# Optimization experiments

Measured on AMD Instinct MI355X. Metric: run time of the kernel, lower is better.

## Reference

```python
import jax, jax.numpy as jnp
import numpy as np

HEAD_SIZE = 128
BLOCK_SIZE = 2048


def setup_inputs() -> dict:
    key = jax.random.key(0)
    kx, kk, kq, kv = jax.random.split(key, 4)
    B, T, C = 8, 2048, HEAD_SIZE
    s = 1.0 / np.sqrt(C)
    x = jax.random.normal(kx, (B, T, C), dtype=jnp.float32)
    Wk = jax.random.normal(kk, (C, C), dtype=jnp.float32) * s
    Wq = jax.random.normal(kq, (C, C), dtype=jnp.float32) * s
    Wv = jax.random.normal(kv, (C, C), dtype=jnp.float32) * s
    return {"x": x, "Wk": Wk, "Wq": Wq, "Wv": Wv}


def reference(x, Wk, Wq, Wv):
    B, T, C = x.shape
    # nn.Linear(C, C, bias=False): y = x @ W.T
    k = jnp.einsum('btc,dc->btd', x, Wk)
    q = jnp.einsum('btc,dc->btd', x, Wq)
    v = jnp.einsum('btc,dc->btd', x, Wv)
    scores = jnp.einsum('btd,bsd->bts', q, k) * (C ** -0.5)  # [B,T,T]
    causal = jnp.tril(jnp.ones((T, T), dtype=bool))
    scores = jnp.where(causal, scores, -jnp.inf)
    weights = jax.nn.softmax(scores, axis=-1)
    return jnp.einsum('bts,bsd->btd', weights, v)
```

## Files before the change

### kernel.cpp

```cpp
#include <hip/hip_runtime.h>

#define T_SEQ 2048
#define C_DIM 128
#define S_QK 0.08838834764831845f

typedef __attribute__((ext_vector_type(8))) short bf16x8;
typedef __attribute__((ext_vector_type(4))) short bf16x4;
typedef __attribute__((ext_vector_type(4))) float f32x4;
typedef __attribute__((ext_vector_type(2))) unsigned int u32x2;

#define OPART_OFF 12582912UL
#define ML_OFF    43778048UL

#define GLOAD_LDS16(gp, lp)                                          \
    __builtin_amdgcn_global_load_lds(                                \
        (const __attribute__((address_space(1))) void*)(gp),         \
        (__attribute__((address_space(3))) void*)(lp), 16, 0, 0)

__device__ __forceinline__ unsigned short f2bf(float f) {
    union { float f; unsigned int u; } v; v.f = f;
    unsigned int r = v.u + 0x7FFFu + ((v.u >> 16) & 1u);
    return (unsigned short)(r >> 16);
}

__device__ __forceinline__ f32x4 mfma16(bf16x4 a, bf16x4 b, f32x4 c) {
    f32x4 d = c;
    asm("v_mfma_f32_16x16x16_bf16 %0, %1, %2, %0" : "+v"(d) : "v"(a), "v"(b));
    return d;
}

__device__ __forceinline__ int base5(int qt) {
    int g = qt / 5 + 1;
    return 5 * g * (g - 1) / 2 + (qt - 5 * (g - 1)) * g;
}

__global__ __launch_bounds__(256) void proj_kernel(
    const float* __restrict__ x,
    const float* __restrict__ Wk, const float* __restrict__ Wq,
    const float* __restrict__ Wv,
    unsigned short* __restrict__ qo, unsigned short* __restrict__ ko,
    unsigned short* __restrict__ vto)
{
    const int rt = blockIdx.x;
    const int z  = blockIdx.y;
    const int tid  = threadIdx.x;
    const int lane = tid & 63;
    const int w    = tid >> 6;
    const int n16  = lane & 15;
    const int quad = lane >> 4;

    __shared__ __align__(16) unsigned short Wl[128 * 136];
    __shared__ __align__(16) unsigned short Xl[9216];

    const float* Wsrc = (z == 0 ? Wq : z == 1 ? Wk : Wv);
    const float wscale = (z == 0) ? S_QK : 1.0f;
    #pragma unroll
    for (int i = 0; i < 16; ++i) {
        int e = (tid + i * 256) * 4;
        int r = e >> 7, c = e & 127;
        float4 v = *reinterpret_cast<const float4*>(Wsrc + e);
        float ax = v.x * wscale, ay = v.y * wscale;
        float az = v.z * wscale, aw = v.w * wscale;
        unsigned lo, hi;
        asm("v_cvt_pk_bf16_f32 %0, %1, %2" : "=v"(lo) : "v"(ax), "v"(ay));
        asm("v_cvt_pk_bf16_f32 %0, %1, %2" : "=v"(hi) : "v"(az), "v"(aw));
        uint2 o2; o2.x = lo; o2.y = hi;
        *reinterpret_cast<uint2*>(&Wl[r * 136 + c]) = o2;
    }
    const float* xrow = x + (size_t)rt * 64 * C_DIM;
    #pragma unroll
    for (int i = 0; i < 8; ++i) {
        int e = (tid + i * 256) * 4;
        int r = e >> 7, c = e & 127;
        float4 v = *reinterpret_cast<const float4*>(xrow + e);
        unsigned lo, hi;
        asm("v_cvt_pk_bf16_f32 %0, %1, %2" : "=v"(lo) : "v"(v.x), "v"(v.y));
        asm("v_cvt_pk_bf16_f32 %0, %1, %2" : "=v"(hi) : "v"(v.z), "v"(v.w));
        uint2 o2; o2.x = lo; o2.y = hi;
        *reinterpret_cast<uint2*>(&Xl[r * 136 + c]) = o2;
    }
    __syncthreads();

    const int arow = w * 16 + n16;
    bf16x8 afr[4];
    #pragma unroll
    for (int kk = 0; kk < 4; ++kk)
        afr[kk] = *reinterpret_cast<const bf16x8*>(&Xl[arow * 136 + kk * 32 + quad * 8]);

    f32x4 acc[8];
    #pragma unroll
    for (int nt = 0; nt < 8; ++nt) acc[nt] = (f32x4){0.f, 0.f, 0.f, 0.f};
    #pragma unroll
    for (int kk = 0; kk < 4; ++kk)
        #pragma unroll
        for (int nt = 0; nt < 8; ++nt) {
            bf16x8 bfr = *reinterpret_cast<const bf16x8*>(
                &Wl[(nt * 16 + n16) * 136 + kk * 32 + quad * 8]);
            acc[nt] = __builtin_amdgcn_mfma_f32_16x16x32_bf16(afr[kk], bfr, acc[nt], 0, 0, 0);
        }

    const int trow_base = w * 16 + quad * 4;
    __syncthreads();
    if (z < 2) {
        #pragma unroll
        for (int nt = 0; nt < 8; ++nt)
            #pragma unroll
            for (int r = 0; r < 4; ++r)
                Xl[(trow_base + r) * 136 + nt * 16 + n16] = f2bf(acc[nt][r]);
        __syncthreads();
        unsigned short* dst = (z == 0 ? qo : ko) + (size_t)rt * 64 * C_DIM;
        #pragma unroll
        for (int i = 0; i < 4; ++i) {
            int e = (tid + i * 256) * 8;
            int r = e >> 7, c = e & 127;
            *reinterpret_cast<uint4*>(dst + e) =
                *reinterpret_cast<const uint4*>(&Xl[r * 136 + c]);
        }
    } else {
        const int b  = rt >> 5;
        const int qt = rt & 31;
        #pragma unroll
        for (int nt = 0; nt < 8; ++nt)
            #pragma unroll
            for (int r = 0; r < 4; ++r)
                Xl[(nt * 16 + n16) * 72 + trow_base + r] = f2bf(acc[nt][r]);
        __syncthreads();
        unsigned short* dst = vto + (size_t)b * C_DIM * T_SEQ + (size_t)qt * 64;
        #pragma unroll
        for (int i = 0; i < 4; ++i) {
            int e = tid + i * 256;
            int d = e >> 3, cv = (e & 7) * 8;
            *reinterpret_cast<uint4*>(dst + (size_t)d * T_SEQ + cv) =
                *reinterpret_cast<const uint4*>(&Xl[d * 72 + cv]);
        }
    }
}

__device__ __forceinline__ void stage_tile32(
    const char* ksb, const char* vsb,
    unsigned short* klbuf, unsigned short* vlbuf, int tid, int w)
{
    #pragma unroll
    for (int it = 0; it < 2; ++it) {
        const int L = it * 256 + tid;
        const int r = L >> 4, c = L & 15;
        GLOAD_LDS16(ksb + r * 256 + ((c ^ (r & 7)) << 4),
                    klbuf + (size_t)(it * 256 + w * 64) * 8);
    }
    #pragma unroll
    for (int it = 0; it < 2; ++it) {
        const int L = it * 256 + tid;
        const int r = L >> 2, c = L & 3;
        GLOAD_LDS16(vsb + (size_t)r * (T_SEQ * 2) +
                        ((c ^ (r & 3) ^ ((r >> 2) & 3)) << 4),
                    vlbuf + (size_t)(it * 256 + w * 64) * 8);
    }
}

__global__ __launch_bounds__(256, 3) void attn_kernel(
    const unsigned short* __restrict__ qb,
    const unsigned short* __restrict__ kb,
    const unsigned short* __restrict__ vtb,
    float* __restrict__ opart, float2* __restrict__ mlbuf,
    float* __restrict__ out)
{
    const int lin = blockIdx.x;
    const int b   = lin & 7;
    const int s   = lin >> 3;
    int g = 1, gbase = 0;
    while (s - gbase >= 5 * g) { gbase += 5 * g; ++g; }
    const int qt    = 5 * (g - 1) + (s - gbase) / g;
    const int chunk = (s - gbase) % g;
    const int nch   = g;

    const int tid  = threadIdx.x;
    const int lane = tid & 63;
    const int w    = tid >> 6;
    const int n16  = lane & 15;
    const int quad = lane >> 4;

    __shared__ __align__(16) unsigned short Kl[2][32 * 128];
    __shared__ __align__(16) unsigned short Vl[2][128 * 32];

    const size_t bT = (size_t)b * T_SEQ;
    const int qbase = qt * 64 + w * 16;
    const int ulim  = 4 * qt + w;

    const int st0 = chunk * 10;
    const int st1 = min(st0 + 10, 2 * qt + 2);

    const char* kbase = (const char*)(kb + bT * C_DIM);
    const char* vbase = (const char*)(vtb + (size_t)b * C_DIM * T_SEQ);

    stage_tile32(kbase + (size_t)st0 * 8192, vbase + (size_t)st0 * 64,
                 Kl[0], Vl[0], tid, w);

    const unsigned short* qp = qb + (bT + qbase + n16) * C_DIM + quad * 8;
    bf16x8 qfr0 = *reinterpret_cast<const bf16x8*>(qp);
    bf16x8 qfr1 = *reinterpret_cast<const bf16x8*>(qp + 32);
    bf16x8 qfr2 = *reinterpret_cast<const bf16x8*>(qp + 64);
    bf16x8 qfr3 = *reinterpret_cast<const bf16x8*>(qp + 96);

    f32x4 o0 = (f32x4){0.f,0.f,0.f,0.f}, o1 = (f32x4){0.f,0.f,0.f,0.f};
    f32x4 o2 = (f32x4){0.f,0.f,0.f,0.f}, o3 = (f32x4){0.f,0.f,0.f,0.f};
    f32x4 o4 = (f32x4){0.f,0.f,0.f,0.f}, o5 = (f32x4){0.f,0.f,0.f,0.f};
    f32x4 o6 = (f32x4){0.f,0.f,0.f,0.f}, o7 = (f32x4){0.f,0.f,0.f,0.f};
    float l_ = 0.f;

    const int kx  = n16 & 7;
    const int sig = (n16 & 3) ^ ((n16 >> 2) & 3);
    const int vof0 = n16 * 32 + (((quad >> 1) ^ sig) << 3) + (quad & 1) * 4;
    const int vof1 = n16 * 32 + ((((quad >> 1) + 2) ^ sig) << 3) + (quad & 1) * 4;

    int cur = 0;
    for (int st = st0; st < st1; ++st, cur ^= 1) {
        if (st + 1 < st1) {
            stage_tile32(kbase + (size_t)(st + 1) * 8192,
                         vbase + (size_t)(st + 1) * 64,
                         Kl[cur ^ 1], Vl[cur ^ 1], tid, w);
            asm volatile("s_waitcnt vmcnt(4)" ::: "memory");
        } else {
            asm volatile("s_waitcnt vmcnt(0)" ::: "memory");
        }
        __builtin_amdgcn_s_barrier();

        const unsigned short* klc = Kl[cur];
        const unsigned short* vlc = Vl[cur];

        #pragma unroll
        for (int sub = 0; sub < 2; ++sub) {
            const int u = st * 2 + sub;
            if (u <= ulim) {
                const unsigned short* krow = klc + (sub * 16 + n16) * 128;
                bf16x8 kf0 = *reinterpret_cast<const bf16x8*>(krow + (((0 + quad) ^ kx) << 3));
                bf16x8 kf1 = *reinterpret_cast<const bf16x8*>(krow + (((4 + quad) ^ kx) << 3));
                bf16x8 kf2 = *reinterpret_cast<const bf16x8*>(krow + (((8 + quad) ^ kx) << 3));
                bf16x8 kf3 = *reinterpret_cast<const bf16x8*>(krow + (((12 + quad) ^ kx) << 3));
                f32x4 s4 = (f32x4){0.f, 0.f, 0.f, 0.f};
                s4 = __builtin_amdgcn_mfma_f32_16x16x32_bf16(kf0, qfr0, s4, 0, 0, 0);
                s4 = __builtin_amdgcn_mfma_f32_16x16x32_bf16(kf1, qfr1, s4, 0, 0, 0);
                s4 = __builtin_amdgcn_mfma_f32_16x16x32_bf16(kf2, qfr2, s4, 0, 0, 0);
                s4 = __builtin_amdgcn_mfma_f32_16x16x32_bf16(kf3, qfr3, s4, 0, 0, 0);

                if (u == ulim) {
                    #pragma unroll
                    for (int r = 0; r < 4; ++r) {
                        int sabs = u * 16 + quad * 4 + r;
                        if (sabs > qbase + n16) s4[r] = -1e30f;
                    }
                }

                float p0 = __expf(s4[0]), p1 = __expf(s4[1]);
                float p2 = __expf(s4[2]), p3 = __expf(s4[3]);
                l_ += (p0 + p1) + (p2 + p3);

                unsigned plo, phi;
                asm("v_cvt_pk_bf16_f32 %0, %1, %2" : "=v"(plo) : "v"(p0), "v"(p1));
                asm("v_cvt_pk_bf16_f32 %0, %1, %2" : "=v"(phi) : "v"(p2), "v"(p3));
                u32x2 pp; pp.x = plo; pp.y = phi;
                bf16x4 pv = __builtin_bit_cast(bf16x4, pp);

                const int vof = sub ? vof1 : vof0;
                o0 = mfma16(*reinterpret_cast<const bf16x4*>(vlc + 0 * 512 + vof), pv, o0);
                o1 = mfma16(*reinterpret_cast<const bf16x4*>(vlc + 1 * 512 + vof), pv, o1);
                o2 = mfma16(*reinterpret_cast<const bf16x4*>(vlc + 2 * 512 + vof), pv, o2);
                o3 = mfma16(*reinterpret_cast<const bf16x4*>(vlc + 3 * 512 + vof), pv, o3);
                o4 = mfma16(*reinterpret_cast<const bf16x4*>(vlc + 4 * 512 + vof), pv, o4);
                o5 = mfma16(*reinterpret_cast<const bf16x4*>(vlc + 5 * 512 + vof), pv, o5);
                o6 = mfma16(*reinterpret_cast<const bf16x4*>(vlc + 6 * 512 + vof), pv, o6);
                o7 = mfma16(*reinterpret_cast<const bf16x4*>(vlc + 7 * 512 + vof), pv, o7);
            }
        }

        asm volatile("s_waitcnt lgkmcnt(0)" ::: "memory");
        __builtin_amdgcn_s_barrier();
    }

    l_ += __shfl_xor(l_, 16);
    l_ += __shfl_xor(l_, 32);

#define STORE4(dst, o, sc)                                            \
    { float4 r4;                                                      \
      r4.x = (o)[0] * (sc); r4.y = (o)[1] * (sc);                     \
      r4.z = (o)[2] * (sc); r4.w = (o)[3] * (sc);                     \
      *reinterpret_cast<float4*>(dst) = r4; }

    if (nch == 1) {
        float* outp = out + (bT + qbase + n16) * C_DIM + quad * 4;
        const float inv = 1.0f / l_;
        STORE4(outp +   0, o0, inv); STORE4(outp +  16, o1, inv);
        STORE4(outp +  32, o2, inv); STORE4(outp +  48, o3, inv);
        STORE4(outp +  64, o4, inv); STORE4(outp +  80, o5, inv);
        STORE4(outp +  96, o6, inv); STORE4(outp + 112, o7, inv);
        return;
    }

    const int slot = b * 119 + s;
    float* op = opart + (size_t)slot * 8192 + (size_t)(w * 16 + n16) * 128 + quad * 4;
    STORE4(op +   0, o0, 1.0f); STORE4(op +  16, o1, 1.0f);
    STORE4(op +  32, o2, 1.0f); STORE4(op +  48, o3, 1.0f);
    STORE4(op +  64, o4, 1.0f); STORE4(op +  80, o5, 1.0f);
    STORE4(op +  96, o6, 1.0f); STORE4(op + 112, o7, 1.0f);
    if (quad == 0)
        mlbuf[(size_t)slot * 64 + w * 16 + n16] = make_float2(0.f, l_);
#undef STORE4
}

__global__ __launch_bounds__(256) void merge_kernel(
    const float* __restrict__ opart, const float2* __restrict__ mlbuf,
    float* __restrict__ out)
{
    const int qt = 5 + blockIdx.x;
    const int b  = blockIdx.y;
    const int nch  = qt / 5 + 1;
    const int base = b * 119 + base5(qt);
    const int row = threadIdx.x >> 2;
    const int c0  = (threadIdx.x & 3) * 32;

    float L = 0.f;
    #pragma unroll
    for (int i = 0; i < 7; ++i)
        if (i < nch) L += mlbuf[(size_t)(base + i) * 64 + row].y;
    const float inv = 1.0f / L;

    float* orow = out + ((size_t)(b * T_SEQ + qt * 64 + row)) * C_DIM;
    #pragma unroll
    for (int j = 0; j < 8; ++j) {
        int col = c0 + j * 4;
        float ax = 0.f, ay = 0.f, az = 0.f, aw = 0.f;
        #pragma unroll
        for (int i = 0; i < 7; ++i) {
            if (i < nch) {
                float4 p = *reinterpret_cast<const float4*>(
                    opart + (size_t)(base + i) * 8192 + row * 128 + col);
                ax += p.x; ay += p.y; az += p.z; aw += p.w;
            }
        }
        float4 r4; r4.x = ax * inv; r4.y = ay * inv; r4.z = az * inv; r4.w = aw * inv;
        *reinterpret_cast<float4*>(orow + col) = r4;
    }
}

extern "C" void kernel_launch(void* const* d_in, const int* in_sizes, int n_in,
                              void* d_out, int out_size, void* d_ws, size_t ws_size,
                              hipStream_t stream) {
    const float* x  = (const float*)d_in[0];
    const float* Wk = (const float*)d_in[1];
    const float* Wq = (const float*)d_in[2];
    const float* Wv = (const float*)d_in[3];

    unsigned short* qw  = (unsigned short*)d_ws;
    unsigned short* kw  = qw + 2097152;
    unsigned short* vw  = kw + 2097152;
    float*          opart = (float*)((char*)d_ws + OPART_OFF);
    float2*         mlb   = (float2*)((char*)d_ws + ML_OFF);

    proj_kernel<<<dim3(256, 3), 256, 0, stream>>>(x, Wk, Wq, Wv, qw, kw, vw);
    attn_kernel<<<dim3(952), 256, 0, stream>>>(qw, kw, vw, opart, mlb, (float*)d_out);
    merge_kernel<<<dim3(27, 8), 256, 0, stream>>>(opart, mlb, (float*)d_out);
}
```

Measured before the change: 116.5 us.

## Double query rows per wave to reuse each staged K/V tile twice

Each wave now handles two 16-row query groups, so a block covers 128 query rows instead of 64. Every K/V tile staged in shared memory and read into registers then feeds twice the MFMA work, halving K/V traffic per query. The split-KV chunking, partial-output slots and merge kernel are recomputed for the new tiling, which also cuts the grid to 488 blocks. In exchange, register pressure roughly doubles (16 accumulators plus 8 Q fragments), which can hurt the 3-blocks-per-SIMD occupancy target, and the causal work is balanced less finely.

New measurement: 126.5 us. 8.6% more time.

```diff
diff --git a/kernel.cpp b/kernel.cpp
--- a/kernel.cpp
+++ b/kernel.cpp
@@ -10,7 +10,7 @@
 typedef __attribute__((ext_vector_type(2))) unsigned int u32x2;
 
 #define OPART_OFF 12582912UL
-#define ML_OFF    43778048UL
+#define ML_OFF    44564480UL
 
 #define GLOAD_LDS16(gp, lp)                                          \
     __builtin_amdgcn_global_load_lds(                                \
@@ -27,11 +27,6 @@
     f32x4 d = c;
     asm("v_mfma_f32_16x16x16_bf16 %0, %1, %2, %0" : "+v"(d) : "v"(a), "v"(b));
     return d;
-}
-
-__device__ __forceinline__ int base5(int qt) {
-    int g = qt / 5 + 1;
-    return 5 * g * (g - 1) / 2 + (qt - 5 * (g - 1)) * g;
 }
 
 __global__ __launch_bounds__(256) void proj_kernel(
@@ -167,11 +162,13 @@
     const int lin = blockIdx.x;
     const int b   = lin & 7;
     const int s   = lin >> 3;
-    int g = 1, gbase = 0;
-    while (s - gbase >= 5 * g) { gbase += 5 * g; ++g; }
-    const int qt    = 5 * (g - 1) + (s - gbase) / g;
-    const int chunk = (s - gbase) % g;
-    const int nch   = g;
+    int qt2 = 0, acc = 0, nch = 1;
+    for (;;) {
+        nch = (4 * qt2 + 13) / 10;
+        if (s < acc + nch) break;
+        acc += nch; ++qt2;
+    }
+    const int chunk = s - acc;
 
     const int tid  = threadIdx.x;
     const int lane = tid & 63;
@@ -183,11 +180,14 @@
     __shared__ __align__(16) unsigned short Vl[2][128 * 32];
 
     const size_t bT = (size_t)b * T_SEQ;
-    const int qbase = qt * 64 + w * 16;
-    const int ulim  = 4 * qt + w;
+    const int qbase = qt2 * 128 + w * 32;
+    const int qrA = qbase + n16;
+    const int qrB = qrA + 16;
+    const int uA = 8 * qt2 + 2 * w;
+    const int uB = uA + 1;
 
     const int st0 = chunk * 10;
-    const int st1 = min(st0 + 10, 2 * qt + 2);
+    const int st1 = min(st0 + 10, 4 * qt2 + 4);
 
     const char* kbase = (const char*)(kb + bT * C_DIM);
     const char* vbase = (const char*)(vtb + (size_t)b * C_DIM * T_SEQ);
@@ -195,17 +195,25 @@
     stage_tile32(kbase + (size_t)st0 * 8192, vbase + (size_t)st0 * 64,
                  Kl[0], Vl[0], tid, w);
 
-    const unsigned short* qp = qb + (bT + qbase + n16) * C_DIM + quad * 8;
-    bf16x8 qfr0 = *reinterpret_cast<const bf16x8*>(qp);
-    bf16x8 qfr1 = *reinterpret_cast<const bf16x8*>(qp + 32);
-    bf16x8 qfr2 = *reinterpret_cast<const bf16x8*>(qp + 64);
-    bf16x8 qfr3 = *reinterpret_cast<const bf16x8*>(qp + 96);
-
-    f32x4 o0 = (f32x4){0.f,0.f,0.f,0.f}, o1 = (f32x4){0.f,0.f,0.f,0.f};
-    f32x4 o2 = (f32x4){0.f,0.f,0.f,0.f}, o3 = (f32x4){0.f,0.f,0.f,0.f};
-    f32x4 o4 = (f32x4){0.f,0.f,0.f,0.f}, o5 = (f32x4){0.f,0.f,0.f,0.f};
-    f32x4 o6 = (f32x4){0.f,0.f,0.f,0.f}, o7 = (f32x4){0.f,0.f,0.f,0.f};
-    float l_ = 0.f;
+    const unsigned short* qp = qb + (bT + qrA) * C_DIM + quad * 8;
+    bf16x8 qfrA0 = *reinterpret_cast<const bf16x8*>(qp);
+    bf16x8 qfrA1 = *reinterpret_cast<const bf16x8*>(qp + 32);
+    bf16x8 qfrA2 = *reinterpret_cast<const bf16x8*>(qp + 64);
+    bf16x8 qfrA3 = *reinterpret_cast<const bf16x8*>(qp + 96);
+    bf16x8 qfrB0 = *reinterpret_cast<const bf16x8*>(qp + 16 * C_DIM);
+    bf16x8 qfrB1 = *reinterpret_cast<const bf16x8*>(qp + 16 * C_DIM + 32);
+    bf16x8 qfrB2 = *reinterpret_cast<const bf16x8*>(qp + 16 * C_DIM + 64);
+    bf16x8 qfrB3 = *reinterpret_cast<const bf16x8*>(qp + 16 * C_DIM + 96);
+
+    f32x4 oA0 = (f32x4){0.f,0.f,0.f,0.f}, oA1 = (f32x4){0.f,0.f,0.f,0.f};
+    f32x4 oA2 = (f32x4){0.f,0.f,0.f,0.f}, oA3 = (f32x4){0.f,0.f,0.f,0.f};
+    f32x4 oA4 = (f32x4){0.f,0.f,0.f,0.f}, oA5 = (f32x4){0.f,0.f,0.f,0.f};
+    f32x4 oA6 = (f32x4){0.f,0.f,0.f,0.f}, oA7 = (f32x4){0.f,0.f,0.f,0.f};
+    f32x4 oB0 = (f32x4){0.f,0.f,0.f,0.f}, oB1 = (f32x4){0.f,0.f,0.f,0.f};
+    f32x4 oB2 = (f32x4){0.f,0.f,0.f,0.f}, oB3 = (f32x4){0.f,0.f,0.f,0.f};
+    f32x4 oB4 = (f32x4){0.f,0.f,0.f,0.f}, oB5 = (f32x4){0.f,0.f,0.f,0.f};
+    f32x4 oB6 = (f32x4){0.f,0.f,0.f,0.f}, oB7 = (f32x4){0.f,0.f,0.f,0.f};
+    float lA = 0.f, lB = 0.f;
 
     const int kx  = n16 & 7;
     const int sig = (n16 & 3) ^ ((n16 >> 2) & 3);
@@ -230,45 +238,68 @@
         #pragma unroll
         for (int sub = 0; sub < 2; ++sub) {
             const int u = st * 2 + sub;
-            if (u <= ulim) {
+            if (u <= uB) {
                 const unsigned short* krow = klc + (sub * 16 + n16) * 128;
                 bf16x8 kf0 = *reinterpret_cast<const bf16x8*>(krow + (((0 + quad) ^ kx) << 3));
                 bf16x8 kf1 = *reinterpret_cast<const bf16x8*>(krow + (((4 + quad) ^ kx) << 3));
                 bf16x8 kf2 = *reinterpret_cast<const bf16x8*>(krow + (((8 + quad) ^ kx) << 3));
                 bf16x8 kf3 = *reinterpret_cast<const bf16x8*>(krow + (((12 + quad) ^ kx) << 3));
-                f32x4 s4 = (f32x4){0.f, 0.f, 0.f, 0.f};
-                s4 = __builtin_amdgcn_mfma_f32_16x16x32_bf16(kf0, qfr0, s4, 0, 0, 0);
-                s4 = __builtin_amdgcn_mfma_f32_16x16x32_bf16(kf1, qfr1, s4, 0, 0, 0);
-                s4 = __builtin_amdgcn_mfma_f32_16x16x32_bf16(kf2, qfr2, s4, 0, 0, 0);
-                s4 = __builtin_amdgcn_mfma_f32_16x16x32_bf16(kf3, qfr3, s4, 0, 0, 0);
-
-                if (u == ulim) {
+                const int vof = sub ? vof1 : vof0;
+                const int sb0 = u * 16 + quad * 4;
+
+                if (u <= uA) {
+                    f32x4 s4 = (f32x4){0.f, 0.f, 0.f, 0.f};
+                    s4 = __builtin_amdgcn_mfma_f32_16x16x32_bf16(kf0, qfrA0, s4, 0, 0, 0);
+                    s4 = __builtin_amdgcn_mfma_f32_16x16x32_bf16(kf1, qfrA1, s4, 0, 0, 0);
+                    s4 = __builtin_amdgcn_mfma_f32_16x16x32_bf16(kf2, qfrA2, s4, 0, 0, 0);
+                    s4 = __builtin_amdgcn_mfma_f32_16x16x32_bf16(kf3, qfrA3, s4, 0, 0, 0);
                     #pragma unroll
-                    for (int r = 0; r < 4; ++r) {
-                        int sabs = u * 16 + quad * 4 + r;
-                        if (sabs > qbase + n16) s4[r] = -1e30f;
-                    }
+                    for (int r = 0; r < 4; ++r)
+                        if (sb0 + r > qrA) s4[r] = -1e30f;
+                    float p0 = __expf(s4[0]), p1 = __expf(s4[1]);
+                    float p2 = __expf(s4[2]), p3 = __expf(s4[3]);
+                    lA += (p0 + p1) + (p2 + p3);
+                    unsigned plo, phi;
+                    asm("v_cvt_pk_bf16_f32 %0, %1, %2" : "=v"(plo) : "v"(p0), "v"(p1));
+                    asm("v_cvt_pk_bf16_f32 %0, %1, %2" : "=v"(phi) : "v"(p2), "v"(p3));
+                    u32x2 pp; pp.x = plo; pp.y = phi;
+                    bf16x4 pv = __builtin_bit_cast(bf16x4, pp);
+                    oA0 = mfma16(*reinterpret_cast<const bf16x4*>(vlc + 0 * 512 + vof), pv, oA0);
+                    oA1 = mfma16(*reinterpret_cast<const bf16x4*>(vlc + 1 * 512 + vof), pv, oA1);
+                    oA2 = mfma16(*reinterpret_cast<const bf16x4*>(vlc + 2 * 512 + vof), pv, oA2);
+                    oA3 = mfma16(*reinterpret_cast<const bf16x4*>(vlc + 3 * 512 + vof), pv, oA3);
+                    oA4 = mfma16(*reinterpret_cast<const bf16x4*>(vlc + 4 * 512 + vof), pv, oA4);
+                    oA5 = mfma16(*reinterpret_cast<const bf16x4*>(vlc + 5 * 512 + vof), pv, oA5);
+                    oA6 = mfma16(*reinterpret_cast<const bf16x4*>(vlc + 6 * 512 + vof), pv, oA6);
+                    oA7 = mfma16(*reinterpret_cast<const bf16x4*>(vlc + 7 * 512 + vof), pv, oA7);
                 }
 
-                float p0 = __expf(s4[0]), p1 = __expf(s4[1]);
-                float p2 = __expf(s4[2]), p3 = __expf(s4[3]);
-                l_ += (p0 + p1) + (p2 + p3);
-
-                unsigned plo, phi;
-                asm("v_cvt_pk_bf16_f32 %0, %1, %2" : "=v"(plo) : "v"(p0), "v"(p1));
-                asm("v_cvt_pk_bf16_f32 %0, %1, %2" : "=v"(phi) : "v"(p2), "v"(p3));
-                u32x2 pp; pp.x = plo; pp.y = phi;
-                bf16x4 pv = __builtin_bit_cast(bf16x4, pp);
-
-                const int vof = sub ? vof1 : vof0;
-                o0 = mfma16(*reinterpret_cast<const bf16x4*>(vlc + 0 * 512 + vof), pv, o0);
-                o1 = mfma16(*reinterpret_cast<const bf16x4*>(vlc + 1 * 512 + vof), pv, o1);
-                o2 = mfma16(*reinterpret_cast<const bf16x4*>(vlc + 2 * 512 + vof), pv, o2);
-                o3 = mfma16(*reinterpret_cast<const bf16x4*>(vlc + 3 * 512 + vof), pv, o3);
-                o4 = mfma16(*reinterpret_cast<const bf16x4*>(vlc + 4 * 512 + vof), pv, o4);
-                o5 = mfma16(*reinterpret_cast<const bf16x4*>(vlc + 5 * 512 + vof), pv, o5);
-                o6 = mfma16(*reinterpret_cast<const bf16x4*>(vlc + 6 * 512 + vof), pv, o6);
-                o7 = mfma16(*reinterpret_cast<const bf16x4*>(vlc + 7 * 512 + vof), pv, o7);
+                {
+                    f32x4 s4 = (f32x4){0.f, 0.f, 0.f, 0.f};
+                    s4 = __builtin_amdgcn_mfma_f32_16x16x32_bf16(kf0, qfrB0, s4, 0, 0, 0);
+                    s4 = __builtin_amdgcn_mfma_f32_16x16x32_bf16(kf1, qfrB1, s4, 0, 0, 0);
+                    s4 = __builtin_amdgcn_mfma_f32_16x16x32_bf16(kf2, qfrB2, s4, 0, 0, 0);
+                    s4 = __builtin_amdgcn_mfma_f32_16x16x32_bf16(kf3, qfrB3, s4, 0, 0, 0);
+                    #pragma unroll
+                    for (int r = 0; r < 4; ++r)
+                        if (sb0 + r > qrB) s4[r] = -1e30f;
+                    float p0 = __expf(s4[0]), p1 = __expf(s4[1]);
+                    float p2 = __expf(s4[2]), p3 = __expf(s4[3]);
+                    lB += (p0 + p1) + (p2 + p3);
+                    unsigned plo, phi;
+                    asm("v_cvt_pk_bf16_f32 %0, %1, %2" : "=v"(plo) : "v"(p0), "v"(p1));
+                    asm("v_cvt_pk_bf16_f32 %0, %1, %2" : "=v"(phi) : "v"(p2), "v"(p3));
+                    u32x2 pp; pp.x = plo; pp.y = phi;
+                    bf16x4 pv = __builtin_bit_cast(bf16x4, pp);
+                    oB0 = mfma16(*reinterpret_cast<const bf16x4*>(vlc + 0 * 512 + vof), pv, oB0);
+                    oB1 = mfma16(*reinterpret_cast<const bf16x4*>(vlc + 1 * 512 + vof), pv, oB1);
+                    oB2 = mfma16(*reinterpret_cast<const bf16x4*>(vlc + 2 * 512 + vof), pv, oB2);
+                    oB3 = mfma16(*reinterpret_cast<const bf16x4*>(vlc + 3 * 512 + vof), pv, oB3);
+                    oB4 = mfma16(*reinterpret_cast<const bf16x4*>(vlc + 4 * 512 + vof), pv, oB4);
+                    oB5 = mfma16(*reinterpret_cast<const bf16x4*>(vlc + 5 * 512 + vof), pv, oB5);
+                    oB6 = mfma16(*reinterpret_cast<const bf16x4*>(vlc + 6 * 512 + vof), pv, oB6);
+                    oB7 = mfma16(*reinterpret_cast<const bf16x4*>(vlc + 7 * 512 + vof), pv, oB7);
+                }
             }
         }
 
@@ -276,8 +307,8 @@
         __builtin_amdgcn_s_barrier();
     }
 
-    l_ += __shfl_xor(l_, 16);
-    l_ += __shfl_xor(l_, 32);
+    lA += __shfl_xor(lA, 16); lA += __shfl_xor(lA, 32);
+    lB += __shfl_xor(lB, 16); lB += __shfl_xor(lB, 32);
 
 #define STORE4(dst, o, sc)                                            \
     { float4 r4;                                                      \
@@ -286,23 +317,36 @@
       *reinterpret_cast<float4*>(dst) = r4; }
 
     if (nch == 1) {
-        float* outp = out + (bT + qbase + n16) * C_DIM + quad * 4;
-        const float inv = 1.0f / l_;
-        STORE4(outp +   0, o0, inv); STORE4(outp +  16, o1, inv);
-        STORE4(outp +  32, o2, inv); STORE4(outp +  48, o3, inv);
-        STORE4(outp +  64, o4, inv); STORE4(outp +  80, o5, inv);
-        STORE4(outp +  96, o6, inv); STORE4(outp + 112, o7, inv);
+        float* oa = out + (bT + qrA) * C_DIM + quad * 4;
+        float* ob = oa + 16 * C_DIM;
+        const float invA = 1.0f / lA, invB = 1.0f / lB;
+        STORE4(oa +   0, oA0, invA); STORE4(oa +  16, oA1, invA);
+        STORE4(oa +  32, oA2, invA); STORE4(oa +  48, oA3, invA);
+        STORE4(oa +  64, oA4, invA); STORE4(oa +  80, oA5, invA);
+        STORE4(oa +  96, oA6, invA); STORE4(oa + 112, oA7, invA);
+        STORE4(ob +   0, oB0, invB); STORE4(ob +  16, oB1, invB);
+        STORE4(ob +  32, oB2, invB); STORE4(ob +  48, oB3, invB);
+        STORE4(ob +  64, oB4, invB); STORE4(ob +  80, oB5, invB);
+        STORE4(ob +  96, oB6, invB); STORE4(ob + 112, oB7, invB);
         return;
     }
 
-    const int slot = b * 119 + s;
-    float* op = opart + (size_t)slot * 8192 + (size_t)(w * 16 + n16) * 128 + quad * 4;
-    STORE4(op +   0, o0, 1.0f); STORE4(op +  16, o1, 1.0f);
-    STORE4(op +  32, o2, 1.0f); STORE4(op +  48, o3, 1.0f);
-    STORE4(op +  64, o4, 1.0f); STORE4(op +  80, o5, 1.0f);
-    STORE4(op +  96, o6, 1.0f); STORE4(op + 112, o7, 1.0f);
-    if (quad == 0)
-        mlbuf[(size_t)slot * 64 + w * 16 + n16] = make_float2(0.f, l_);
+    const int slot = b * 61 + s;
+    float* opa = opart + (size_t)slot * 16384
+                 + (size_t)(w * 32 + n16) * 128 + quad * 4;
+    float* opb = opa + 16 * 128;
+    STORE4(opa +   0, oA0, 1.0f); STORE4(opa +  16, oA1, 1.0f);
+    STORE4(opa +  32, oA2, 1.0f); STORE4(opa +  48, oA3, 1.0f);
+    STORE4(opa +  64, oA4, 1.0f); STORE4(opa +  80, oA5, 1.0f);
+    STORE4(opa +  96, oA6, 1.0f); STORE4(opa + 112, oA7, 1.0f);
+    STORE4(opb +   0, oB0, 1.0f); STORE4(opb +  16, oB1, 1.0f);
+    STORE4(opb +  32, oB2, 1.0f); STORE4(opb +  48, oB3, 1.0f);
+    STORE4(opb +  64, oB4, 1.0f); STORE4(opb +  80, oB5, 1.0f);
+    STORE4(opb +  96, oB6, 1.0f); STORE4(opb + 112, oB7, 1.0f);
+    if (quad == 0) {
+        mlbuf[(size_t)slot * 128 + w * 32 + n16]      = make_float2(0.f, lA);
+        mlbuf[(size_t)slot * 128 + w * 32 + 16 + n16] = make_float2(0.f, lB);
+    }
 #undef STORE4
 }
 
@@ -310,29 +354,31 @@
     const float* __restrict__ opart, const float2* __restrict__ mlbuf,
     float* __restrict__ out)
 {
-    const int qt = 5 + blockIdx.x;
-    const int b  = blockIdx.y;
-    const int nch  = qt / 5 + 1;
-    const int base = b * 119 + base5(qt);
-    const int row = threadIdx.x >> 2;
-    const int c0  = (threadIdx.x & 3) * 32;
+    const int qt2 = 2 + blockIdx.x;
+    const int b   = blockIdx.y;
+    const int nch = (4 * qt2 + 13) / 10;
+    int sb = 0;
+    for (int j = 0; j < qt2; ++j) sb += (4 * j + 13) / 10;
+    const int base = b * 61 + sb;
+    const int row = threadIdx.x >> 1;
+    const int c0  = (threadIdx.x & 1) * 64;
 
     float L = 0.f;
     #pragma unroll
     for (int i = 0; i < 7; ++i)
-        if (i < nch) L += mlbuf[(size_t)(base + i) * 64 + row].y;
+        if (i < nch) L += mlbuf[(size_t)(base + i) * 128 + row].y;
     const float inv = 1.0f / L;
 
-    float* orow = out + ((size_t)(b * T_SEQ + qt * 64 + row)) * C_DIM;
-    #pragma unroll
-    for (int j = 0; j < 8; ++j) {
+    float* orow = out + ((size_t)(b * T_SEQ + qt2 * 128 + row)) * C_DIM;
+    #pragma unroll
+    for (int j = 0; j < 16; ++j) {
         int col = c0 + j * 4;
         float ax = 0.f, ay = 0.f, az = 0.f, aw = 0.f;
         #pragma unroll
         for (int i = 0; i < 7; ++i) {
             if (i < nch) {
                 float4 p = *reinterpret_cast<const float4*>(
-                    opart + (size_t)(base + i) * 8192 + row * 128 + col);
+                    opart + (size_t)(base + i) * 16384 + row * 128 + col);
                 ax += p.x; ay += p.y; az += p.z; aw += p.w;
             }
         }
@@ -356,6 +402,6 @@
     float2*         mlb   = (float2*)((char*)d_ws + ML_OFF);
 
     proj_kernel<<<dim3(256, 3), 256, 0, stream>>>(x, Wk, Wq, Wv, qw, kw, vw);
-    attn_kernel<<<dim3(952), 256, 0, stream>>>(qw, kw, vw, opart, mlb, (float*)d_out);
-    merge_kernel<<<dim3(27, 8), 256, 0, stream>>>(opart, mlb, (float*)d_out);
-}
+    attn_kernel<<<dim3(488), 256, 0, stream>>>(qw, kw, vw, opart, mlb, (float*)d_out);
+    merge_kernel<<<dim3(14, 8), 256, 0, stream>>>(opart, mlb, (float*)d_out);
+}
```

## Switch attention to single-wave 16-row blocks with 16-tile KV split chunks

Applied to the files above, without the earlier changes.

Attention now runs as 64-thread workgroups, each handling 16 query rows, instead of 256-thread blocks covering 64 rows with four waves. KV is consumed in 16-key tiles double-buffered per wave, and work is split into chunks of up to 16 tiles, giving 4608 blocks. This removes block-wide barriers and the idle waves left by causal imbalance. In exchange, each K/V tile is staged per wave rather than shared across four waves, and there are more partial outputs to merge.

Result: slower. 130.3 us (+11.9%).

```diff
diff --git a/kernel.cpp b/kernel.cpp
--- a/kernel.cpp
+++ b/kernel.cpp
@@ -10,7 +10,7 @@
 typedef __attribute__((ext_vector_type(2))) unsigned int u32x2;
 
 #define OPART_OFF 12582912UL
-#define ML_OFF    43778048UL
+#define ML_OFF    50331648UL
 
 #define GLOAD_LDS16(gp, lp)                                          \
     __builtin_amdgcn_global_load_lds(                                \
@@ -27,11 +27,6 @@
     f32x4 d = c;
     asm("v_mfma_f32_16x16x16_bf16 %0, %1, %2, %0" : "+v"(d) : "v"(a), "v"(b));
     return d;
-}
-
-__device__ __forceinline__ int base5(int qt) {
-    int g = qt / 5 + 1;
-    return 5 * g * (g - 1) / 2 + (qt - 5 * (g - 1)) * g;
 }
 
 __global__ __launch_bounds__(256) void proj_kernel(
@@ -136,28 +131,27 @@
     }
 }
 
-__device__ __forceinline__ void stage_tile32(
+__device__ __forceinline__ void stage16(
     const char* ksb, const char* vsb,
-    unsigned short* klbuf, unsigned short* vlbuf, int tid, int w)
+    unsigned short* kl, unsigned short* vl, int tid)
 {
     #pragma unroll
-    for (int it = 0; it < 2; ++it) {
-        const int L = it * 256 + tid;
+    for (int it = 0; it < 4; ++it) {
+        const int L = it * 64 + tid;
         const int r = L >> 4, c = L & 15;
         GLOAD_LDS16(ksb + r * 256 + ((c ^ (r & 7)) << 4),
-                    klbuf + (size_t)(it * 256 + w * 64) * 8);
-    }
-    #pragma unroll
-    for (int it = 0; it < 2; ++it) {
-        const int L = it * 256 + tid;
-        const int r = L >> 2, c = L & 3;
-        GLOAD_LDS16(vsb + (size_t)r * (T_SEQ * 2) +
-                        ((c ^ (r & 3) ^ ((r >> 2) & 3)) << 4),
-                    vlbuf + (size_t)(it * 256 + w * 64) * 8);
-    }
-}
-
-__global__ __launch_bounds__(256, 3) void attn_kernel(
+                    kl + (size_t)(it * 64) * 8);
+    }
+    #pragma unroll
+    for (int it = 0; it < 4; ++it) {
+        const int L = it * 64 + tid;
+        const int r = L >> 1, c = L & 1;
+        GLOAD_LDS16(vsb + (size_t)r * (T_SEQ * 2) + ((c ^ (r & 1)) << 4),
+                    vl + (size_t)(it * 64) * 8);
+    }
+}
+
+__global__ __launch_bounds__(64, 3) void attn_kernel(
     const unsigned short* __restrict__ qb,
     const unsigned short* __restrict__ kb,
     const unsigned short* __restrict__ vtb,
@@ -167,35 +161,32 @@
     const int lin = blockIdx.x;
     const int b   = lin & 7;
     const int s   = lin >> 3;
-    int g = 1, gbase = 0;
-    while (s - gbase >= 5 * g) { gbase += 5 * g; ++g; }
-    const int qt    = 5 * (g - 1) + (s - gbase) / g;
-    const int chunk = (s - gbase) % g;
-    const int nch   = g;
+    int g = 0;
+    while (s >= 8 * (g + 1) * (g + 2)) ++g;
+    const int rem   = s - 8 * g * (g + 1);
+    const int qi    = 16 * g + rem / (g + 1);
+    const int chunk = rem % (g + 1);
+    const int nch   = g + 1;
 
     const int tid  = threadIdx.x;
-    const int lane = tid & 63;
-    const int w    = tid >> 6;
-    const int n16  = lane & 15;
-    const int quad = lane >> 4;
-
-    __shared__ __align__(16) unsigned short Kl[2][32 * 128];
-    __shared__ __align__(16) unsigned short Vl[2][128 * 32];
+    const int n16  = tid & 15;
+    const int quad = tid >> 4;
+
+    __shared__ __align__(16) unsigned short Kl[2][16 * 128];
+    __shared__ __align__(16) unsigned short Vl[2][128 * 16];
 
     const size_t bT = (size_t)b * T_SEQ;
-    const int qbase = qt * 64 + w * 16;
-    const int ulim  = 4 * qt + w;
-
-    const int st0 = chunk * 10;
-    const int st1 = min(st0 + 10, 2 * qt + 2);
+    const int qr = qi * 16 + n16;
+    const int u0 = chunk * 16;
+    const int u1 = min(u0 + 16, qi + 1);
 
     const char* kbase = (const char*)(kb + bT * C_DIM);
     const char* vbase = (const char*)(vtb + (size_t)b * C_DIM * T_SEQ);
 
-    stage_tile32(kbase + (size_t)st0 * 8192, vbase + (size_t)st0 * 64,
-                 Kl[0], Vl[0], tid, w);
-
-    const unsigned short* qp = qb + (bT + qbase + n16) * C_DIM + quad * 8;
+    stage16(kbase + (size_t)u0 * 4096, vbase + (size_t)u0 * 32,
+            Kl[0], Vl[0], tid);
+
+    const unsigned short* qp = qb + (bT + qr) * C_DIM + quad * 8;
     bf16x8 qfr0 = *reinterpret_cast<const bf16x8*>(qp);
     bf16x8 qfr1 = *reinterpret_cast<const bf16x8*>(qp + 32);
     bf16x8 qfr2 = *reinterpret_cast<const bf16x8*>(qp + 64);
@@ -208,72 +199,55 @@
     float l_ = 0.f;
 
     const int kx  = n16 & 7;
-    const int sig = (n16 & 3) ^ ((n16 >> 2) & 3);
-    const int vof0 = n16 * 32 + (((quad >> 1) ^ sig) << 3) + (quad & 1) * 4;
-    const int vof1 = n16 * 32 + ((((quad >> 1) + 2) ^ sig) << 3) + (quad & 1) * 4;
+    const int vof = n16 * 16 + ((((quad >> 1) ^ (n16 & 1))) << 3) + (quad & 1) * 4;
 
     int cur = 0;
-    for (int st = st0; st < st1; ++st, cur ^= 1) {
-        if (st + 1 < st1) {
-            stage_tile32(kbase + (size_t)(st + 1) * 8192,
-                         vbase + (size_t)(st + 1) * 64,
-                         Kl[cur ^ 1], Vl[cur ^ 1], tid, w);
-            asm volatile("s_waitcnt vmcnt(4)" ::: "memory");
+    for (int u = u0; u < u1; ++u, cur ^= 1) {
+        if (u + 1 < u1) {
+            stage16(kbase + (size_t)(u + 1) * 4096, vbase + (size_t)(u + 1) * 32,
+                    Kl[cur ^ 1], Vl[cur ^ 1], tid);
+            asm volatile("s_waitcnt vmcnt(8)" ::: "memory");
         } else {
             asm volatile("s_waitcnt vmcnt(0)" ::: "memory");
         }
-        __builtin_amdgcn_s_barrier();
 
         const unsigned short* klc = Kl[cur];
         const unsigned short* vlc = Vl[cur];
 
-        #pragma unroll
-        for (int sub = 0; sub < 2; ++sub) {
-            const int u = st * 2 + sub;
-            if (u <= ulim) {
-                const unsigned short* krow = klc + (sub * 16 + n16) * 128;
-                bf16x8 kf0 = *reinterpret_cast<const bf16x8*>(krow + (((0 + quad) ^ kx) << 3));
-                bf16x8 kf1 = *reinterpret_cast<const bf16x8*>(krow + (((4 + quad) ^ kx) << 3));
-                bf16x8 kf2 = *reinterpret_cast<const bf16x8*>(krow + (((8 + quad) ^ kx) << 3));
-                bf16x8 kf3 = *reinterpret_cast<const bf16x8*>(krow + (((12 + quad) ^ kx) << 3));
-                f32x4 s4 = (f32x4){0.f, 0.f, 0.f, 0.f};
-                s4 = __builtin_amdgcn_mfma_f32_16x16x32_bf16(kf0, qfr0, s4, 0, 0, 0);
-                s4 = __builtin_amdgcn_mfma_f32_16x16x32_bf16(kf1, qfr1, s4, 0, 0, 0);
-                s4 = __builtin_amdgcn_mfma_f32_16x16x32_bf16(kf2, qfr2, s4, 0, 0, 0);
-                s4 = __builtin_amdgcn_mfma_f32_16x16x32_bf16(kf3, qfr3, s4, 0, 0, 0);
-
-                if (u == ulim) {
-                    #pragma unroll
-                    for (int r = 0; r < 4; ++r) {
-                        int sabs = u * 16 + quad * 4 + r;
-                        if (sabs > qbase + n16) s4[r] = -1e30f;
-                    }
-                }
-
-                float p0 = __expf(s4[0]), p1 = __expf(s4[1]);
-                float p2 = __expf(s4[2]), p3 = __expf(s4[3]);
-                l_ += (p0 + p1) + (p2 + p3);
-
-                unsigned plo, phi;
-                asm("v_cvt_pk_bf16_f32 %0, %1, %2" : "=v"(plo) : "v"(p0), "v"(p1));
-                asm("v_cvt_pk_bf16_f32 %0, %1, %2" : "=v"(phi) : "v"(p2), "v"(p3));
-                u32x2 pp; pp.x = plo; pp.y = phi;
-                bf16x4 pv = __builtin_bit_cast(bf16x4, pp);
-
-                const int vof = sub ? vof1 : vof0;
-                o0 = mfma16(*reinterpret_cast<const bf16x4*>(vlc + 0 * 512 + vof), pv, o0);
-                o1 = mfma16(*reinterpret_cast<const bf16x4*>(vlc + 1 * 512 + vof), pv, o1);
-                o2 = mfma16(*reinterpret_cast<const bf16x4*>(vlc + 2 * 512 + vof), pv, o2);
-                o3 = mfma16(*reinterpret_cast<const bf16x4*>(vlc + 3 * 512 + vof), pv, o3);
-                o4 = mfma16(*reinterpret_cast<const bf16x4*>(vlc + 4 * 512 + vof), pv, o4);
-                o5 = mfma16(*reinterpret_cast<const bf16x4*>(vlc + 5 * 512 + vof), pv, o5);
-                o6 = mfma16(*reinterpret_cast<const bf16x4*>(vlc + 6 * 512 + vof), pv, o6);
-                o7 = mfma16(*reinterpret_cast<const bf16x4*>(vlc + 7 * 512 + vof), pv, o7);
-            }
-        }
-
-        asm volatile("s_waitcnt lgkmcnt(0)" ::: "memory");
-        __builtin_amdgcn_s_barrier();
+        const unsigned short* krow = klc + n16 * 128;
+        bf16x8 kf0 = *reinterpret_cast<const bf16x8*>(krow + (((0  + quad) ^ kx) << 3));
+        bf16x8 kf1 = *reinterpret_cast<const bf16x8*>(krow + (((4  + quad) ^ kx) << 3));
+        bf16x8 kf2 = *reinterpret_cast<const bf16x8*>(krow + (((8  + quad) ^ kx) << 3));
+        bf16x8 kf3 = *reinterpret_cast<const bf16x8*>(krow + (((12 + quad) ^ kx) << 3));
+        f32x4 s4 = (f32x4){0.f, 0.f, 0.f, 0.f};
+        s4 = __builtin_amdgcn_mfma_f32_16x16x32_bf16(kf0, qfr0, s4, 0, 0, 0);
+        s4 = __builtin_amdgcn_mfma_f32_16x16x32_bf16(kf1, qfr1, s4, 0, 0, 0);
+        s4 = __builtin_amdgcn_mfma_f32_16x16x32_bf16(kf2, qfr2, s4, 0, 0, 0);
+        s4 = __builtin_amdgcn_mfma_f32_16x16x32_bf16(kf3, qfr3, s4, 0, 0, 0);
+
+        const int sb0 = u * 16 + quad * 4;
+        #pragma unroll
+        for (int r = 0; r < 4; ++r)
+            if (sb0 + r > qr) s4[r] = -1e30f;
+
+        float p0 = __expf(s4[0]), p1 = __expf(s4[1]);
+        float p2 = __expf(s4[2]), p3 = __expf(s4[3]);
+        l_ += (p0 + p1) + (p2 + p3);
+
+        unsigned plo, phi;
+        asm("v_cvt_pk_bf16_f32 %0, %1, %2" : "=v"(plo) : "v"(p0), "v"(p1));
+        asm("v_cvt_pk_bf16_f32 %0, %1, %2" : "=v"(phi) : "v"(p2), "v"(p3));
+        u32x2 pp; pp.x = plo; pp.y = phi;
+        bf16x4 pv = __builtin_bit_cast(bf16x4, pp);
+
+        o0 = mfma16(*reinterpret_cast<const bf16x4*>(vlc + 0 * 256 + vof), pv, o0);
+        o1 = mfma16(*reinterpret_cast<const bf16x4*>(vlc + 1 * 256 + vof), pv, o1);
+        o2 = mfma16(*reinterpret_cast<const bf16x4*>(vlc + 2 * 256 + vof), pv, o2);
+        o3 = mfma16(*reinterpret_cast<const bf16x4*>(vlc + 3 * 256 + vof), pv, o3);
+        o4 = mfma16(*reinterpret_cast<const bf16x4*>(vlc + 4 * 256 + vof), pv, o4);
+        o5 = mfma16(*reinterpret_cast<const bf16x4*>(vlc + 5 * 256 + vof), pv, o5);
+        o6 = mfma16(*reinterpret_cast<const bf16x4*>(vlc + 6 * 256 + vof), pv, o6);
+        o7 = mfma16(*reinterpret_cast<const bf16x4*>(vlc + 7 * 256 + vof), pv, o7);
     }
 
     l_ += __shfl_xor(l_, 16);
@@ -286,7 +260,7 @@
       *reinterpret_cast<float4*>(dst) = r4; }
 
     if (nch == 1) {
-        float* outp = out + (bT + qbase + n16) * C_DIM + quad * 4;
+        float* outp = out + (bT + qr) * C_DIM + quad * 4;
         const float inv = 1.0f / l_;
         STORE4(outp +   0, o0, inv); STORE4(outp +  16, o1, inv);
         STORE4(outp +  32, o2, inv); STORE4(outp +  48, o3, inv);
@@ -295,14 +269,14 @@
         return;
     }
 
-    const int slot = b * 119 + s;
-    float* op = opart + (size_t)slot * 8192 + (size_t)(w * 16 + n16) * 128 + quad * 4;
+    const int slot = b * 576 + s;
+    float* op = opart + (size_t)slot * 2048 + (size_t)n16 * 128 + quad * 4;
     STORE4(op +   0, o0, 1.0f); STORE4(op +  16, o1, 1.0f);
     STORE4(op +  32, o2, 1.0f); STORE4(op +  48, o3, 1.0f);
     STORE4(op +  64, o4, 1.0f); STORE4(op +  80, o5, 1.0f);
     STORE4(op +  96, o6, 1.0f); STORE4(op + 112, o7, 1.0f);
     if (quad == 0)
-        mlbuf[(size_t)slot * 64 + w * 16 + n16] = make_float2(0.f, l_);
+        mlbuf[(size_t)slot * 16 + n16] = make_float2(0.f, l_);
 #undef STORE4
 }
 
@@ -310,29 +284,31 @@
     const float* __restrict__ opart, const float2* __restrict__ mlbuf,
     float* __restrict__ out)
 {
-    const int qt = 5 + blockIdx.x;
+    const int qi = 16 + blockIdx.x;
     const int b  = blockIdx.y;
-    const int nch  = qt / 5 + 1;
-    const int base = b * 119 + base5(qt);
-    const int row = threadIdx.x >> 2;
-    const int c0  = (threadIdx.x & 3) * 32;
+    const int g  = qi >> 4;
+    const int nch  = g + 1;
+    const int sb   = 8 * g * (g + 1) + (qi & 15) * (g + 1);
+    const int base = b * 576 + sb;
+    const int row = threadIdx.x >> 4;
+    const int c0  = (threadIdx.x & 15) * 8;
 
     float L = 0.f;
     #pragma unroll
-    for (int i = 0; i < 7; ++i)
-        if (i < nch) L += mlbuf[(size_t)(base + i) * 64 + row].y;
+    for (int i = 0; i < 8; ++i)
+        if (i < nch) L += mlbuf[(size_t)(base + i) * 16 + row].y;
     const float inv = 1.0f / L;
 
-    float* orow = out + ((size_t)(b * T_SEQ + qt * 64 + row)) * C_DIM;
-    #pragma unroll
-    for (int j = 0; j < 8; ++j) {
+    float* orow = out + ((size_t)(b * T_SEQ + qi * 16 + row)) * C_DIM;
+    #pragma unroll
+    for (int j = 0; j < 2; ++j) {
         int col = c0 + j * 4;
         float ax = 0.f, ay = 0.f, az = 0.f, aw = 0.f;
         #pragma unroll
-        for (int i = 0; i < 7; ++i) {
+        for (int i = 0; i < 8; ++i) {
             if (i < nch) {
                 float4 p = *reinterpret_cast<const float4*>(
-                    opart + (size_t)(base + i) * 8192 + row * 128 + col);
+                    opart + (size_t)(base + i) * 2048 + row * 128 + col);
                 ax += p.x; ay += p.y; az += p.z; aw += p.w;
             }
         }
@@ -356,6 +332,6 @@
     float2*         mlb   = (float2*)((char*)d_ws + ML_OFF);
 
     proj_kernel<<<dim3(256, 3), 256, 0, stream>>>(x, Wk, Wq, Wv, qw, kw, vw);
-    attn_kernel<<<dim3(952), 256, 0, stream>>>(qw, kw, vw, opart, mlb, (float*)d_out);
-    merge_kernel<<<dim3(27, 8), 256, 0, stream>>>(opart, mlb, (float*)d_out);
-}
+    attn_kernel<<<dim3(4608), 64, 0, stream>>>(qw, kw, vw, opart, mlb, (float*)d_out);
+    merge_kernel<<<dim3(112, 8), 256, 0, stream>>>(opart, mlb, (float*)d_out);
+}
```
